# Optimization experiments

Hardware: AMD Instinct MI355X
Metric: run time of the kernel (lower is better)

## Reference

```python
import jax, jax.numpy as jnp
import numpy as np

B, I, H = 16384, 512, 512


def setup_inputs() -> dict:
    key = jax.random.key(0)
    ks = jax.random.split(key, 6)
    scale_s = 1.0 / np.sqrt(H + I + 1)
    scale_g = 1.0 / np.sqrt(H + I + H)
    return {
        "x_t": jax.random.normal(ks[0], (B, I), dtype=jnp.float32),
        "delta_t": jax.random.uniform(ks[1], (B, 1), dtype=jnp.float32),
        "h_prev": jax.random.normal(ks[2], (B, H), dtype=jnp.float32),
        "c_prev": jax.random.normal(ks[3], (B, H), dtype=jnp.float32),
        # linear_s: in = H + I + 1
        "Ws": jax.random.normal(ks[4], (H + I + 1, H), dtype=jnp.float32) * scale_s,
        "bs": jnp.zeros((H,), dtype=jnp.float32),
        # stacked weights for the 5 gates (f, i, T, u, o), each in = H + I + H
        "Wg": jax.random.normal(ks[5], (2 * H + I, 5 * H), dtype=jnp.float32) * scale_g,
        "bg": jnp.zeros((5 * H,), dtype=jnp.float32),
    }


def reference(x_t, delta_t, h_prev, c_prev, Ws, bs, Wg, bg):
    # time gate: s_t = tanh(Linear([h_prev, x_t, delta_t]))
    s_t = jnp.tanh(jnp.concatenate([h_prev, x_t, delta_t], axis=1) @ Ws + bs)
    # shared-input GEMM for the 5 gates on concat([h_prev, x_t, s_t])
    z = jnp.concatenate([h_prev, x_t, s_t], axis=1) @ Wg + bg  # [B, 5H]
    f_t = jax.nn.sigmoid(z[:, 0 * H:1 * H])
    i_t = jax.nn.sigmoid(z[:, 1 * H:2 * H])
    T_t = jax.nn.sigmoid(z[:, 2 * H:3 * H])
    zeta_t = jnp.tanh(z[:, 3 * H:4 * H])
    o_t = jax.nn.sigmoid(z[:, 4 * H:5 * H])
    c_t = f_t * c_prev + i_t * zeta_t + T_t * s_t
    h_t = o_t * jnp.tanh(c_t)
    return (h_t, c_t)
```

## Files before the change

### kernel.cpp

```cpp
#include <hip/hip_runtime.h>
#include <stdint.h>
#include <stddef.h>

#define Bsz 16384
#define Hsz 512
#define KG 1536
#define KA 1024
#define NT 48

typedef float f32x4 __attribute__((ext_vector_type(4)));
typedef short bf16x8 __attribute__((ext_vector_type(8)));
typedef unsigned short u16;
typedef unsigned int u32;

__device__ __forceinline__ u16 f2bf(float f) {
  union { float f; unsigned u; } v; v.f = f;
  return (u16)((v.u + 0x7fffu + ((v.u >> 16) & 1u)) >> 16);
}
__device__ __forceinline__ float bf2f(u16 h) {
  union { unsigned u; float f; } v; v.u = ((unsigned)h) << 16;
  return v.f;
}
__device__ __forceinline__ float sigm(float x) {
  return 1.0f / (1.0f + __expf(-x));
}
__device__ __forceinline__ float tanh_(float x) {
  x = fminf(fmaxf(x, -15.0f), 15.0f);
  float e = __expf(2.0f * x);
  return (e - 1.0f) / (e + 1.0f);
}

__device__ __forceinline__ void gload_lds16(const u16* g, u16* l) {
  __builtin_amdgcn_global_load_lds(
      (__attribute__((address_space(1))) void*)(g),
      (__attribute__((address_space(3))) void*)(l), 16, 0, 0);
}

#define VMCNT(n) asm volatile("s_waitcnt vmcnt(" #n ")" ::: "memory")

__global__ __launch_bounds__(256) void prep_A_kernel(
    const float* __restrict__ h_prev, const float* __restrict__ x_t,
    u16* __restrict__ A) {
  const int b = blockIdx.x;
  const int q = threadIdx.x;
  const int qq = q & 127;
  const float4* src = (q < 128) ? (const float4*)h_prev : (const float4*)x_t;
  float4 v = src[(size_t)b * 128 + qq];
  ushort4 o;
  o.x = f2bf(v.x); o.y = f2bf(v.y); o.z = f2bf(v.z); o.w = f2bf(v.w);
  *(ushort4*)(A + (size_t)b * KG + (size_t)q * 4) = o;
}

__global__ __launch_bounds__(256) void transpose_cast_kernel(
    const float* __restrict__ in, u16* __restrict__ out, int R, int C) {
  __shared__ float tile[32][33];
  const int c0 = blockIdx.x * 32;
  const int r0 = blockIdx.y * 32;
  const int tx = threadIdx.x;
  const int ty = threadIdx.y;
  #pragma unroll
  for (int i = ty; i < 32; i += 8)
    tile[i][tx] = in[(size_t)(r0 + i) * C + (c0 + tx)];
  __syncthreads();
  #pragma unroll
  for (int i = ty; i < 32; i += 8)
    out[(size_t)(c0 + i) * R + (r0 + tx)] = f2bf(tile[tx][i]);
}

__global__ __launch_bounds__(256, 2) void gemm1_kernel(
    const u16* __restrict__ A, const u16* __restrict__ Wst,
    const float* __restrict__ Ws, const float* __restrict__ bs,
    const float* __restrict__ delta, u16* __restrict__ Aout) {
  __shared__ __attribute__((aligned(16))) u16 Als[128][32];
  __shared__ __attribute__((aligned(16))) u16 Bls[128][32];
  const int t = threadIdx.x;
  const int w = t >> 6, l = t & 63;
  const int bm0 = blockIdx.y * 128;
  const int bn0 = blockIdx.x * 128;
  const int wm = w >> 1, wn = w & 1;

  f32x4 zv = {0.f, 0.f, 0.f, 0.f};
  f32x4 acc[4][4];
  #pragma unroll
  for (int i = 0; i < 4; ++i)
    #pragma unroll
    for (int j = 0; j < 4; ++j) acc[i][j] = zv;

  const int r = t >> 2, q = t & 3;
  const u16* gA0 = A + (size_t)(bm0 + r) * KG + q * 8;
  const u16* gA1 = A + (size_t)(bm0 + 64 + r) * KG + q * 8;
  const u16* gB0 = Wst + (size_t)(bn0 + r) * KA + q * 8;
  const u16* gB1 = Wst + (size_t)(bn0 + 64 + r) * KA + q * 8;
  u16* lA0 = &Als[0][0] + w * 512;
  u16* lA1 = &Als[0][0] + 2048 + w * 512;
  u16* lB0 = &Bls[0][0] + w * 512;
  u16* lB1 = &Bls[0][0] + 2048 + w * 512;

  const int frow = l & 15;
  const int kofs = (l >> 4) * 8;

  for (int kt = 0; kt < KA / 32; ++kt) {
    const int ko = kt * 32;
    gload_lds16(gA0 + ko, lA0);
    gload_lds16(gA1 + ko, lA1);
    gload_lds16(gB0 + ko, lB0);
    gload_lds16(gB1 + ko, lB1);
    __syncthreads();
    bf16x8 af[4], bfv[4];
    #pragma unroll
    for (int mi = 0; mi < 4; ++mi)
      af[mi] = *(const bf16x8*)&Als[wm * 64 + mi * 16 + frow][kofs];
    #pragma unroll
    for (int ni = 0; ni < 4; ++ni)
      bfv[ni] = *(const bf16x8*)&Bls[wn * 64 + ni * 16 + frow][kofs];
    #pragma unroll
    for (int mi = 0; mi < 4; ++mi)
      #pragma unroll
      for (int ni = 0; ni < 4; ++ni)
        acc[mi][ni] = __builtin_amdgcn_mfma_f32_16x16x32_bf16(
            af[mi], bfv[ni], acc[mi][ni], 0, 0, 0);
    __syncthreads();
  }

  #pragma unroll
  for (int ni = 0; ni < 4; ++ni) {
    const int col = bn0 + wn * 64 + ni * 16 + (l & 15);
    const float wsl = Ws[(size_t)1024 * 512 + col];
    const float bsv = bs[col];
    #pragma unroll
    for (int mi = 0; mi < 4; ++mi) {
      #pragma unroll
      for (int rr = 0; rr < 4; ++rr) {
        const int row = bm0 + wm * 64 + mi * 16 + (l >> 4) * 4 + rr;
        const float z = acc[mi][ni][rr] + delta[row] * wsl + bsv;
        Aout[(size_t)row * KG + 1024 + col] = f2bf(tanh_(z));
      }
    }
  }
}

__global__ __launch_bounds__(512, 2) void gemm2_8ph(
    const u16* __restrict__ A, const u16* __restrict__ Wgt,
    const float* __restrict__ bg, const float* __restrict__ c_prev,
    float* __restrict__ out) {
  __shared__ __attribute__((aligned(16))) u16 LDSA[4][256 * 32];
  __shared__ __attribute__((aligned(16))) u16 LDSB[4][320 * 32];

  const int t5 = threadIdx.x;
  const int w = t5 >> 6;
  const int l = t5 & 63;

  const int bid = blockIdx.x;
  const int hb = bid & 7;
  const int rb = bid >> 3;
  const int bm0 = rb * 256;
  const int h0 = hb * 64;

  const bool isA = (w < 4);

  const u16* gs0 = nullptr; const u16* gs1 = nullptr; const u16* gs2 = nullptr;
  const u16* gs3 = nullptr; const u16* gs4 = nullptr;
  u32 lo0 = 0, lo1 = 0, lo2 = 0, lo3 = 0, lo4 = 0;

  if (isA) {
#define MKA(s, gp, lo) { int idx = w * 256 + (s) * 64 + l; int row = idx >> 2; \
    int ch = (idx & 3) ^ ((idx >> 3) & 3); \
    gp = A + (size_t)(bm0 + row) * KG + ch * 8; lo = (u32)(w * 256 + (s) * 64) * 8; }
    MKA(0, gs0, lo0) MKA(1, gs1, lo1) MKA(2, gs2, lo2) MKA(3, gs3, lo3)
#undef MKA
  } else {
#define MKB(s, gp, lo) { int idx = (w - 4) * 320 + (s) * 64 + l; int rbw = idx >> 2; \
    int ch = (idx & 3) ^ ((idx >> 3) & 3); \
    int g = rbw >> 6; int hl = rbw & 63; \
    gp = Wgt + (size_t)(g * Hsz + h0 + hl) * KG + ch * 8; \
    lo = (u32)((w - 4) * 320 + (s) * 64) * 8; }
    MKB(0, gs0, lo0) MKB(1, gs1, lo1) MKB(2, gs2, lo2) MKB(3, gs3, lo3) MKB(4, gs4, lo4)
#undef MKB
  }

#define STAGE(kt) { const int _b = (kt) & 3; \
    if (isA) { \
      gload_lds16(gs0 + (size_t)(kt) * 32, &LDSA[_b][lo0]); \
      gload_lds16(gs1 + (size_t)(kt) * 32, &LDSA[_b][lo1]); \
      gload_lds16(gs2 + (size_t)(kt) * 32, &LDSA[_b][lo2]); \
      gload_lds16(gs3 + (size_t)(kt) * 32, &LDSA[_b][lo3]); \
    } else { \
      gload_lds16(gs0 + (size_t)(kt) * 32, &LDSB[_b][lo0]); \
      gload_lds16(gs1 + (size_t)(kt) * 32, &LDSB[_b][lo1]); \
      gload_lds16(gs2 + (size_t)(kt) * 32, &LDSB[_b][lo2]); \
      gload_lds16(gs3 + (size_t)(kt) * 32, &LDSB[_b][lo3]); \
      gload_lds16(gs4 + (size_t)(kt) * 32, &LDSB[_b][lo4]); \
    } }

  f32x4 zv = {0.f, 0.f, 0.f, 0.f};
  f32x4 acc[8][5];
  #pragma unroll
  for (int mi = 0; mi < 8; ++mi)
    #pragma unroll
    for (int g = 0; g < 5; ++g) acc[mi][g] = zv;

  STAGE(0) STAGE(1) STAGE(2)

  const int wm = w >> 2;
  const int wn = w & 3;
  const int frow = l & 15;
  const int kq = l >> 4;
  const u32 axor = (u32)((kq ^ ((frow >> 1) & 3)) << 3);
  const u32 abase = (u32)(wm * 128 + frow) * 32 + axor;
  const u32 bbase = (u32)(wn * 16 + frow) * 32 + axor;

  for (int t = 0; t < NT; ++t) {
    const int rem = NT - 1 - t;
    if (rem >= 3) STAGE(t + 3)
    if (isA) {
      if (rem >= 3) VMCNT(12); else if (rem == 2) VMCNT(8);
      else if (rem == 1) VMCNT(4); else VMCNT(0);
    } else {
      if (rem >= 3) VMCNT(15); else if (rem == 2) VMCNT(10);
      else if (rem == 1) VMCNT(5); else VMCNT(0);
    }
    __builtin_amdgcn_s_barrier();
    asm volatile("" ::: "memory");

    const int bt = t & 3;
    const u16* As = &LDSA[bt][0];
    const u16* Bs = &LDSB[bt][0];
    bf16x8 af[8];
    #pragma unroll
    for (int mi = 0; mi < 8; ++mi)
      af[mi] = *(const bf16x8*)&As[abase + mi * 512];
    __builtin_amdgcn_s_setprio(1);
    #pragma unroll
    for (int g = 0; g < 5; ++g) {
      bf16x8 bf = *(const bf16x8*)&Bs[bbase + g * 2048];
      #pragma unroll
      for (int mi = 0; mi < 8; ++mi)
        acc[mi][g] = __builtin_amdgcn_mfma_f32_16x16x32_bf16(
            af[mi], bf, acc[mi][g], 0, 0, 0);
    }
    __builtin_amdgcn_s_setprio(0);
    asm volatile("" ::: "memory");
    __builtin_amdgcn_s_barrier();
  }
#undef STAGE

  const int hc = h0 + wn * 16 + frow;
  const float b_f = bg[hc];
  const float b_i = bg[Hsz + hc];
  const float b_T = bg[2 * Hsz + hc];
  const float b_z = bg[3 * Hsz + hc];
  const float b_o = bg[4 * Hsz + hc];
  #pragma unroll
  for (int mi = 0; mi < 8; ++mi) {
    #pragma unroll
    for (int rr = 0; rr < 4; ++rr) {
      const int row = bm0 + wm * 128 + mi * 16 + kq * 4 + rr;
      const float fg = sigm(acc[mi][0][rr] + b_f);
      const float ig = sigm(acc[mi][1][rr] + b_i);
      const float Tg = sigm(acc[mi][2][rr] + b_T);
      const float zg = tanh_(acc[mi][3][rr] + b_z);
      const float og = sigm(acc[mi][4][rr] + b_o);
      const float cp = c_prev[(size_t)row * Hsz + hc];
      const float st = bf2f(A[(size_t)row * KG + 1024 + hc]);
      const float c = fg * cp + ig * zg + Tg * st;
      const float h = og * tanh_(c);
      out[(size_t)row * Hsz + hc] = h;
      out[(size_t)Bsz * Hsz + (size_t)row * Hsz + hc] = c;
    }
  }
}

extern "C" void kernel_launch(void* const* d_in, const int* in_sizes, int n_in,
                              void* d_out, int out_size, void* d_ws, size_t ws_size,
                              hipStream_t stream) {
  const float* x_t    = (const float*)d_in[0];
  const float* delta  = (const float*)d_in[1];
  const float* h_prev = (const float*)d_in[2];
  const float* c_prev = (const float*)d_in[3];
  const float* Ws     = (const float*)d_in[4];
  const float* bs     = (const float*)d_in[5];
  const float* Wg     = (const float*)d_in[6];
  const float* bg     = (const float*)d_in[7];
  float* out = (float*)d_out;

  char* wsb = (char*)d_ws;
  u16* A   = (u16*)(wsb);
  u16* Wst = (u16*)(wsb + (size_t)50331648);
  u16* Wgt = (u16*)(wsb + (size_t)51380224);

  prep_A_kernel<<<dim3(16384), dim3(256), 0, stream>>>(h_prev, x_t, A);
  transpose_cast_kernel<<<dim3(16, 32), dim3(32, 8), 0, stream>>>(Ws, Wst, 1024, 512);
  transpose_cast_kernel<<<dim3(80, 48), dim3(32, 8), 0, stream>>>(Wg, Wgt, 1536, 2560);
  gemm1_kernel<<<dim3(4, 128), dim3(256), 0, stream>>>(A, Wst, Ws, bs, delta, A);
  gemm2_8ph<<<dim3(512), dim3(512), 0, stream>>>(A, Wgt, bg, c_prev, out);
}
```

Before: 209.9 us.

## Software-pipeline LDS fragment reads with MFMA in gate GEMM main loop

Restructures the gemm2 K-loop so LDS fragment reads for the next tile and the second A-half are issued with inline ds_read_b128 while the current MFMAs run, using double-buffered B fragment registers and one barrier per tile instead of two. The aim is to hide LDS read latency behind matrix-core work and drop a barrier per iteration. It adds register pressure from the extra fragment sets and relies on hand-placed lgkmcnt/vmcnt waits, which could stall or spill if scheduling goes wrong.

```diff
diff --git a/kernel.cpp b/kernel.cpp
--- a/kernel.cpp
+++ b/kernel.cpp
@@ -6,7 +6,7 @@
 #define Hsz 512
 #define KG 1536
 #define KA 1024
-#define NT 48
+#define NT3 48
 
 typedef float f32x4 __attribute__((ext_vector_type(4)));
 typedef short bf16x8 __attribute__((ext_vector_type(8)));
@@ -36,7 +36,17 @@
       (__attribute__((address_space(3))) void*)(l), 16, 0, 0);
 }
 
+__device__ __forceinline__ bf16x8 ds_read128(u32 byte_addr) {
+  bf16x8 r;
+  asm volatile("ds_read_b128 %0, %1" : "=v"(r) : "v"(byte_addr));
+  return r;
+}
+
 #define VMCNT(n) asm volatile("s_waitcnt vmcnt(" #n ")" ::: "memory")
+#define LGKM0() { asm volatile("s_waitcnt lgkmcnt(0)" ::: "memory"); \
+                  __builtin_amdgcn_sched_barrier(0); }
+#define BAR() { asm volatile("" ::: "memory"); __builtin_amdgcn_s_barrier(); \
+                asm volatile("" ::: "memory"); }
 
 __global__ __launch_bounds__(256) void prep_A_kernel(
     const float* __restrict__ h_prev, const float* __restrict__ x_t,
@@ -139,7 +149,7 @@
   }
 }
 
-__global__ __launch_bounds__(512, 2) void gemm2_8ph(
+__global__ __launch_bounds__(512, 2) void gemm2_pp(
     const u16* __restrict__ A, const u16* __restrict__ Wgt,
     const float* __restrict__ bg, const float* __restrict__ c_prev,
     float* __restrict__ out) {
@@ -199,50 +209,76 @@
     #pragma unroll
     for (int g = 0; g < 5; ++g) acc[mi][g] = zv;
 
-  STAGE(0) STAGE(1) STAGE(2)
-
   const int wm = w >> 2;
   const int wn = w & 3;
   const int frow = l & 15;
   const int kq = l >> 4;
   const u32 axor = (u32)((kq ^ ((frow >> 1) & 3)) << 3);
-  const u32 abase = (u32)(wm * 128 + frow) * 32 + axor;
-  const u32 bbase = (u32)(wn * 16 + frow) * 32 + axor;
-
-  for (int t = 0; t < NT; ++t) {
-    const int rem = NT - 1 - t;
-    if (rem >= 3) STAGE(t + 3)
-    if (isA) {
-      if (rem >= 3) VMCNT(12); else if (rem == 2) VMCNT(8);
-      else if (rem == 1) VMCNT(4); else VMCNT(0);
-    } else {
-      if (rem >= 3) VMCNT(15); else if (rem == 2) VMCNT(10);
-      else if (rem == 1) VMCNT(5); else VMCNT(0);
-    }
-    __builtin_amdgcn_s_barrier();
-    asm volatile("" ::: "memory");
-
-    const int bt = t & 3;
-    const u16* As = &LDSA[bt][0];
-    const u16* Bs = &LDSB[bt][0];
-    bf16x8 af[8];
-    #pragma unroll
-    for (int mi = 0; mi < 8; ++mi)
-      af[mi] = *(const bf16x8*)&As[abase + mi * 512];
-    __builtin_amdgcn_s_setprio(1);
-    #pragma unroll
-    for (int g = 0; g < 5; ++g) {
-      bf16x8 bf = *(const bf16x8*)&Bs[bbase + g * 2048];
-      #pragma unroll
-      for (int mi = 0; mi < 8; ++mi)
-        acc[mi][g] = __builtin_amdgcn_mfma_f32_16x16x32_bf16(
-            af[mi], bf, acc[mi][g], 0, 0, 0);
-    }
-    __builtin_amdgcn_s_setprio(0);
-    asm volatile("" ::: "memory");
-    __builtin_amdgcn_s_barrier();
-  }
+  const u32 abyte = ((u32)(wm * 128 + frow) * 32 + axor) * 2;
+  const u32 bbyte = ((u32)(wn * 16 + frow) * 32 + axor) * 2;
+  const u32 ldsA0 = (u32)(uintptr_t)&LDSA[0][0];
+  const u32 ldsB0 = (u32)(uintptr_t)&LDSB[0][0];
+
+  bf16x8 afH0[4], afH1[4], bfvA[5], bfvB[5];
+
+#define READ9(tt, SET) { \
+    const u32 _aB = ldsA0 + (u32)((tt) & 3) * 16384 + abyte; \
+    const u32 _bB = ldsB0 + (u32)((tt) & 3) * 20480 + bbyte; \
+    afH0[0] = ds_read128(_aB); \
+    afH0[1] = ds_read128(_aB + 1024); \
+    afH0[2] = ds_read128(_aB + 2048); \
+    afH0[3] = ds_read128(_aB + 3072); \
+    SET[0] = ds_read128(_bB); \
+    SET[1] = ds_read128(_bB + 4096); \
+    SET[2] = ds_read128(_bB + 8192); \
+    SET[3] = ds_read128(_bB + 12288); \
+    SET[4] = ds_read128(_bB + 16384); }
+
+#define READH1(tt) { \
+    const u32 _aB = ldsA0 + (u32)((tt) & 3) * 16384 + abyte; \
+    afH1[0] = ds_read128(_aB + 4096); \
+    afH1[1] = ds_read128(_aB + 5120); \
+    afH1[2] = ds_read128(_aB + 6144); \
+    afH1[3] = ds_read128(_aB + 7168); }
+
+#define MFMA20(base, AF, BV) { \
+    __builtin_amdgcn_s_setprio(1); \
+    _Pragma("unroll") \
+    for (int g = 0; g < 5; ++g) { \
+      _Pragma("unroll") \
+      for (int mi = 0; mi < 4; ++mi) \
+        acc[(base) + mi][g] = __builtin_amdgcn_mfma_f32_16x16x32_bf16( \
+            AF[mi], BV[g], acc[(base) + mi][g], 0, 0, 0); \
+    } \
+    __builtin_amdgcn_s_setprio(0); }
+
+#define TILE(t, CUR, NXT) { \
+    LGKM0();                           \
+    READH1(t)                          \
+    if ((t) + 3 < NT3) STAGE((t) + 3) \
+    MFMA20(0, afH0, CUR) \
+    LGKM0();                           \
+    if ((t) + 3 < NT3) { if (isA) { VMCNT(8); } else { VMCNT(10); } } \
+    else if ((t) + 2 < NT3) { if (isA) { VMCNT(4); } else { VMCNT(5); } } \
+    else { VMCNT(0); } \
+    BAR();                             \
+    if ((t) + 1 < NT3) READ9((t) + 1, NXT)   \
+    MFMA20(4, afH1, CUR) }
+
+  STAGE(0) STAGE(1) STAGE(2)
+  if (isA) { VMCNT(8); } else { VMCNT(10); }
+  BAR();
+  READ9(0, bfvA)
+
+  for (int t2 = 0; t2 < NT3; t2 += 2) {
+    TILE(t2, bfvA, bfvB)
+    TILE(t2 + 1, bfvB, bfvA)
+  }
+#undef TILE
 #undef STAGE
+#undef READ9
+#undef READH1
+#undef MFMA20
 
   const int hc = h0 + wn * 16 + frow;
   const float b_f = bg[hc];
@@ -292,5 +328,5 @@
   transpose_cast_kernel<<<dim3(16, 32), dim3(32, 8), 0, stream>>>(Ws, Wst, 1024, 512);
   transpose_cast_kernel<<<dim3(80, 48), dim3(32, 8), 0, stream>>>(Wg, Wgt, 1536, 2560);
   gemm1_kernel<<<dim3(4, 128), dim3(256), 0, stream>>>(A, Wst, Ws, bs, delta, A);
-  gemm2_8ph<<<dim3(512), dim3(512), 0, stream>>>(A, Wgt, bg, c_prev, out);
-}
+  gemm2_pp<<<dim3(512), dim3(512), 0, stream>>>(A, Wgt, bg, c_prev, out);
+}
```

Result: slower. 269.4 us (+28.3%).

## Switch gate GEMM to 32x32x16 MFMA with software-pipelined LDS reads

Applied to the files above, without the earlier changes.

Reworks the gate GEMM kernel to use 32x32x16 bf16 MFMA tiles instead of 16x16x32, rearranging the 8 waves as a 4x2 grid, each computing 64 rows by 32 columns across the 5 gates. LDS fragment reads become inline-asm ds_read_b128 split into two k-halves. They are double-buffered so the reads for one half overlap the MFMAs of the other, with explicit lgkmcnt waits and a single barrier per iteration. The LDS swizzle changes from XOR to a rotate to match the new read pattern. The intent is fewer LDS reads per MFMA and better latency hiding, at the cost of more complex manual synchronization.

```diff
diff --git a/kernel.cpp b/kernel.cpp
--- a/kernel.cpp
+++ b/kernel.cpp
@@ -6,9 +6,10 @@
 #define Hsz 512
 #define KG 1536
 #define KA 1024
-#define NT 48
+#define NT3 48
 
 typedef float f32x4 __attribute__((ext_vector_type(4)));
+typedef float f32x16 __attribute__((ext_vector_type(16)));
 typedef short bf16x8 __attribute__((ext_vector_type(8)));
 typedef unsigned short u16;
 typedef unsigned int u32;
@@ -37,6 +38,12 @@
 }
 
 #define VMCNT(n) asm volatile("s_waitcnt vmcnt(" #n ")" ::: "memory")
+#define LGKM(n) { asm volatile("s_waitcnt lgkmcnt(" #n ")" ::: "memory"); \
+                  __builtin_amdgcn_sched_barrier(0); }
+#define BAR() { asm volatile("" ::: "memory"); __builtin_amdgcn_s_barrier(); \
+                asm volatile("" ::: "memory"); }
+#define DSR(dst, addr, off) \
+  asm volatile("ds_read_b128 %0, %1 offset:" #off : "=v"(dst) : "v"(addr));
 
 __global__ __launch_bounds__(256) void prep_A_kernel(
     const float* __restrict__ h_prev, const float* __restrict__ x_t,
@@ -139,7 +146,7 @@
   }
 }
 
-__global__ __launch_bounds__(512, 2) void gemm2_8ph(
+__global__ __launch_bounds__(512, 2) void gemm2_32(
     const u16* __restrict__ A, const u16* __restrict__ Wgt,
     const float* __restrict__ bg, const float* __restrict__ c_prev,
     float* __restrict__ out) {
@@ -164,15 +171,15 @@
 
   if (isA) {
 #define MKA(s, gp, lo) { int idx = w * 256 + (s) * 64 + l; int row = idx >> 2; \
-    int ch = (idx & 3) ^ ((idx >> 3) & 3); \
-    gp = A + (size_t)(bm0 + row) * KG + ch * 8; lo = (u32)(w * 256 + (s) * 64) * 8; }
+    int gch = ((idx & 3) + 4 - ((row >> 1) & 3)) & 3; \
+    gp = A + (size_t)(bm0 + row) * KG + gch * 8; lo = (u32)(w * 256 + (s) * 64) * 8; }
     MKA(0, gs0, lo0) MKA(1, gs1, lo1) MKA(2, gs2, lo2) MKA(3, gs3, lo3)
 #undef MKA
   } else {
-#define MKB(s, gp, lo) { int idx = (w - 4) * 320 + (s) * 64 + l; int rbw = idx >> 2; \
-    int ch = (idx & 3) ^ ((idx >> 3) & 3); \
-    int g = rbw >> 6; int hl = rbw & 63; \
-    gp = Wgt + (size_t)(g * Hsz + h0 + hl) * KG + ch * 8; \
+#define MKB(s, gp, lo) { int idx = (w - 4) * 320 + (s) * 64 + l; int brow = idx >> 2; \
+    int gch = ((idx & 3) + 4 - ((brow >> 1) & 3)) & 3; \
+    int g = brow >> 6; int hl = brow & 63; \
+    gp = Wgt + (size_t)(g * Hsz + h0 + hl) * KG + gch * 8; \
     lo = (u32)((w - 4) * 320 + (s) * 64) * 8; }
     MKB(0, gs0, lo0) MKB(1, gs1, lo1) MKB(2, gs2, lo2) MKB(3, gs3, lo3) MKB(4, gs4, lo4)
 #undef MKB
@@ -192,74 +199,97 @@
       gload_lds16(gs4 + (size_t)(kt) * 32, &LDSB[_b][lo4]); \
     } }
 
-  f32x4 zv = {0.f, 0.f, 0.f, 0.f};
-  f32x4 acc[8][5];
-  #pragma unroll
-  for (int mi = 0; mi < 8; ++mi)
-    #pragma unroll
-    for (int g = 0; g < 5; ++g) acc[mi][g] = zv;
+  f32x16 acc[2][5];
+  #pragma unroll
+  for (int mb = 0; mb < 2; ++mb)
+    #pragma unroll
+    for (int g = 0; g < 5; ++g)
+      #pragma unroll
+      for (int e = 0; e < 16; ++e) acc[mb][g][e] = 0.f;
+
+  const int wm = w >> 1;
+  const int wn = w & 1;
+  const int l31 = l & 31;
+  const int lh = l >> 5;
+  const int srow = (l31 >> 1) & 3;
+  const int sch0 = (0 + lh + srow) & 3;
+  const int sch1 = (2 + lh + srow) & 3;
+  const u32 aoff0 = (u32)((wm * 64 + l31) * 64 + sch0 * 16);
+  const u32 aoff1 = (u32)((wm * 64 + l31) * 64 + sch1 * 16);
+  const u32 boff0 = (u32)((wn * 32 + l31) * 64 + sch0 * 16);
+  const u32 boff1 = (u32)((wn * 32 + l31) * 64 + sch1 * 16);
+  const u32 ldsA0 = (u32)(uintptr_t)&LDSA[0][0];
+  const u32 ldsB0 = (u32)(uintptr_t)&LDSB[0][0];
+
+  bf16x8 afA[2], afB[2], bfvA[5], bfvB[5];
+
+#define READ_C0(tt, AF, BV) { \
+    const u32 _a = ldsA0 + (u32)((tt) & 3) * 16384 + aoff0; \
+    const u32 _bb = ldsB0 + (u32)((tt) & 3) * 20480 + boff0; \
+    DSR(AF[0], _a, 0)      DSR(AF[1], _a, 2048) \
+    DSR(BV[0], _bb, 0)     DSR(BV[1], _bb, 4096) \
+    DSR(BV[2], _bb, 8192)  DSR(BV[3], _bb, 12288) \
+    DSR(BV[4], _bb, 16384) }
+#define READ_C1(tt, AF, BV) { \
+    const u32 _a = ldsA0 + (u32)((tt) & 3) * 16384 + aoff1; \
+    const u32 _bb = ldsB0 + (u32)((tt) & 3) * 20480 + boff1; \
+    DSR(AF[0], _a, 0)      DSR(AF[1], _a, 2048) \
+    DSR(BV[0], _bb, 0)     DSR(BV[1], _bb, 4096) \
+    DSR(BV[2], _bb, 8192)  DSR(BV[3], _bb, 12288) \
+    DSR(BV[4], _bb, 16384) }
+#define CLUSTER(AF, BV) { \
+    __builtin_amdgcn_s_setprio(1); \
+    _Pragma("unroll") \
+    for (int g = 0; g < 5; ++g) { \
+      acc[0][g] = __builtin_amdgcn_mfma_f32_32x32x16_bf16( \
+          AF[0], BV[g], acc[0][g], 0, 0, 0); \
+      acc[1][g] = __builtin_amdgcn_mfma_f32_32x32x16_bf16( \
+          AF[1], BV[g], acc[1][g], 0, 0, 0); \
+    } \
+    __builtin_amdgcn_s_setprio(0); }
 
   STAGE(0) STAGE(1) STAGE(2)
-
-  const int wm = w >> 2;
-  const int wn = w & 3;
-  const int frow = l & 15;
-  const int kq = l >> 4;
-  const u32 axor = (u32)((kq ^ ((frow >> 1) & 3)) << 3);
-  const u32 abase = (u32)(wm * 128 + frow) * 32 + axor;
-  const u32 bbase = (u32)(wn * 16 + frow) * 32 + axor;
-
-  for (int t = 0; t < NT; ++t) {
-    const int rem = NT - 1 - t;
-    if (rem >= 3) STAGE(t + 3)
-    if (isA) {
-      if (rem >= 3) VMCNT(12); else if (rem == 2) VMCNT(8);
-      else if (rem == 1) VMCNT(4); else VMCNT(0);
+  if (isA) { VMCNT(8); } else { VMCNT(10); }
+  BAR();
+  READ_C0(0, afA, bfvA)
+
+  for (int t = 0; t < NT3; ++t) {
+    LGKM(0);
+    READ_C1(t, afB, bfvB)
+    CLUSTER(afA, bfvA)
+    if (t + 2 < NT3) { if (isA) { VMCNT(4); } else { VMCNT(5); } }
+    else { VMCNT(0); }
+    BAR();
+    if (t + 3 < NT3) STAGE(t + 3)
+    if (t + 1 < NT3) {
+      READ_C0(t + 1, afA, bfvA)
+      LGKM(7);
     } else {
-      if (rem >= 3) VMCNT(15); else if (rem == 2) VMCNT(10);
-      else if (rem == 1) VMCNT(5); else VMCNT(0);
+      LGKM(0);
     }
-    __builtin_amdgcn_s_barrier();
-    asm volatile("" ::: "memory");
-
-    const int bt = t & 3;
-    const u16* As = &LDSA[bt][0];
-    const u16* Bs = &LDSB[bt][0];
-    bf16x8 af[8];
-    #pragma unroll
-    for (int mi = 0; mi < 8; ++mi)
-      af[mi] = *(const bf16x8*)&As[abase + mi * 512];
-    __builtin_amdgcn_s_setprio(1);
-    #pragma unroll
-    for (int g = 0; g < 5; ++g) {
-      bf16x8 bf = *(const bf16x8*)&Bs[bbase + g * 2048];
-      #pragma unroll
-      for (int mi = 0; mi < 8; ++mi)
-        acc[mi][g] = __builtin_amdgcn_mfma_f32_16x16x32_bf16(
-            af[mi], bf, acc[mi][g], 0, 0, 0);
-    }
-    __builtin_amdgcn_s_setprio(0);
-    asm volatile("" ::: "memory");
-    __builtin_amdgcn_s_barrier();
+    CLUSTER(afB, bfvB)
   }
 #undef STAGE
-
-  const int hc = h0 + wn * 16 + frow;
+#undef READ_C0
+#undef READ_C1
+#undef CLUSTER
+
+  const int hc = h0 + wn * 32 + l31;
   const float b_f = bg[hc];
   const float b_i = bg[Hsz + hc];
   const float b_T = bg[2 * Hsz + hc];
   const float b_z = bg[3 * Hsz + hc];
   const float b_o = bg[4 * Hsz + hc];
   #pragma unroll
-  for (int mi = 0; mi < 8; ++mi) {
-    #pragma unroll
-    for (int rr = 0; rr < 4; ++rr) {
-      const int row = bm0 + wm * 128 + mi * 16 + kq * 4 + rr;
-      const float fg = sigm(acc[mi][0][rr] + b_f);
-      const float ig = sigm(acc[mi][1][rr] + b_i);
-      const float Tg = sigm(acc[mi][2][rr] + b_T);
-      const float zg = tanh_(acc[mi][3][rr] + b_z);
-      const float og = sigm(acc[mi][4][rr] + b_o);
+  for (int mb = 0; mb < 2; ++mb) {
+    #pragma unroll
+    for (int r = 0; r < 16; ++r) {
+      const int row = bm0 + wm * 64 + mb * 32 + (r & 3) + 8 * (r >> 2) + 4 * lh;
+      const float fg = sigm(acc[mb][0][r] + b_f);
+      const float ig = sigm(acc[mb][1][r] + b_i);
+      const float Tg = sigm(acc[mb][2][r] + b_T);
+      const float zg = tanh_(acc[mb][3][r] + b_z);
+      const float og = sigm(acc[mb][4][r] + b_o);
       const float cp = c_prev[(size_t)row * Hsz + hc];
       const float st = bf2f(A[(size_t)row * KG + 1024 + hc]);
       const float c = fg * cp + ig * zg + Tg * st;
@@ -292,5 +322,5 @@
   transpose_cast_kernel<<<dim3(16, 32), dim3(32, 8), 0, stream>>>(Ws, Wst, 1024, 512);
   transpose_cast_kernel<<<dim3(80, 48), dim3(32, 8), 0, stream>>>(Wg, Wgt, 1536, 2560);
   gemm1_kernel<<<dim3(4, 128), dim3(256), 0, stream>>>(A, Wst, Ws, bs, delta, A);
-  gemm2_8ph<<<dim3(512), dim3(512), 0, stream>>>(A, Wgt, bg, c_prev, out);
-}
+  gemm2_32<<<dim3(512), dim3(512), 0, stream>>>(A, Wgt, bg, c_prev, out);
+}
```

New measurement: 210.3 us. No clear change (+0.2%).
